# Kernel optimization log

Hardware: AMD Instinct MI355X
Metric: run time of the kernel (lower is better)

The kernel has to match this reference:

```python
import jax, jax.numpy as jnp
import numpy as np

BINS = 10
LOSS_WEIGHT = 1.0


def setup_inputs() -> dict:
    key = jax.random.key(0)
    k1, k2 = jax.random.split(key)
    B, N = 32, 500000
    pred = jax.random.normal(k1, (B, N), dtype=jnp.float32)
    target = jax.random.randint(k2, (B, N), 0, 2).astype(jnp.float32)
    return {"pred": pred, "target": target}


def reference(pred, target):
    bins = BINS
    # edges = [0, 1/bins, ..., 1], last edge bumped by 1e-6 so g==1 falls in last bin
    edges = jnp.arange(bins + 1, dtype=jnp.float32) / bins
    edges = edges.at[-1].add(1e-6)
    tot = target.shape[1]  # python int, matches target.size(1)

    # gradient magnitude proxy; pred.sigmoid() is detached in the original
    g = jnp.abs(jax.lax.stop_gradient(jax.nn.sigmoid(pred)) - jax.lax.stop_gradient(target))

    # single-pass binning replacing the per-bin python loop:
    # inds_i = (g >= edges[i]) & (g < edges[i+1])  <=>  searchsorted(edges, g, 'right') - 1 == i
    idx = jnp.clip(jnp.searchsorted(edges, g.ravel(), side="right") - 1, 0, bins - 1)
    counts = jnp.bincount(idx, length=bins)  # [bins] int
    n = jnp.sum(counts > 0)                  # number of non-empty bins

    cnt_per_elem = counts[idx].astype(pred.dtype)  # count of the bin each element falls in (>=1)
    w = tot / cnt_per_elem                          # weights[inds] = tot / num_in_bins
    w = jnp.where(n > 0, w / n.astype(pred.dtype), w)
    w = jax.lax.stop_gradient(w.reshape(pred.shape))

    # weighted BCE-with-logits, stable form, reduction='sum', divided by tot
    x = pred
    bce = jnp.maximum(x, 0.0) - x * target + jnp.log1p(jnp.exp(-jnp.abs(x)))
    loss = jnp.sum(w * bce) / tot
    return loss * LOSS_WEIGHT
```

## Files before the change

### kernel.cpp

```cpp
#include <hip/hip_runtime.h>
#include <hip/hip_fp16.h>

#define BINS 10

typedef float f32x4 __attribute__((ext_vector_type(4)));

__device__ __forceinline__ unsigned pk_add_f16x2(unsigned a, unsigned b) {
    __half2 ha = __builtin_bit_cast(__half2, a);
    __half2 hb = __builtin_bit_cast(__half2, b);
    return __builtin_bit_cast(unsigned, __hadd2(ha, hb));
}

__device__ __forceinline__ void ghm_elem(float x, float tt,
                                         unsigned long long& pk,
                                         unsigned (&acc)[5]) {
    float t = __expf(-fabsf(x));
    float u = 1.f + t;
    float r = __builtin_amdgcn_rcpf(u);
    float sig = (x >= 0.f) ? r : t * r;
    float d = sig - tt;
    int idx = (int)(fabsf(d) * 10.f);
    idx = idx < 9 ? idx : 9;
    pk += 1ull << (6 * idx);
    float bce = fmaxf(x, 0.f) - x * tt + __logf(u);
    unsigned hv = (unsigned)__builtin_bit_cast(unsigned short, __float2half(bce));
    hv <<= ((idx & 1) << 4);
    const int pair = idx >> 1;
#pragma unroll
    for (int p = 0; p < 5; ++p)
        acc[p] = pk_add_f16x2(acc[p], (pair == p) ? hv : 0u);
}

__global__ __launch_bounds__(256) void ghm_pass1(
    const float* __restrict__ pred, const float* __restrict__ tgt,
    long long n, int nb,
    float* __restrict__ bsum, int* __restrict__ bcnt)
{
    __shared__ float rsum[4][BINS];
    __shared__ int   rcnt[4][BINS];

    const int tid  = threadIdx.x;
    const int lane = tid & 63;
    const int wave = tid >> 6;

    float s[BINS];
#pragma unroll
    for (int b = 0; b < BINS; ++b) s[b] = 0.f;
    unsigned acc[5];
#pragma unroll
    for (int p = 0; p < 5; ++p) acc[p] = 0u;
    unsigned long long pk = 0;
    int c[BINS];
#pragma unroll
    for (int b = 0; b < BINS; ++b) c[b] = 0;

    const long long n4 = n >> 2;
    const f32x4* p4 = (const f32x4*)pred;
    const f32x4* t4 = (const f32x4*)tgt;

    const long long qpb = (n4 + nb - 1) / nb;
    const long long q0  = (long long)blockIdx.x * qpb;
    const long long q1  = (q0 + qpb < n4) ? (q0 + qpb) : n4;

    int chunk = 0;
    for (long long i = q0 + tid; i < q1; i += 512) {
        f32x4 pa = __builtin_nontemporal_load(&p4[i]);
        f32x4 ta = __builtin_nontemporal_load(&t4[i]);
        const long long j = i + 256;
        f32x4 pb, tb;
        const bool has2 = (j < q1);
        if (has2) {
            pb = __builtin_nontemporal_load(&p4[j]);
            tb = __builtin_nontemporal_load(&t4[j]);
        }
        ghm_elem(pa.x, ta.x, pk, acc);
        ghm_elem(pa.y, ta.y, pk, acc);
        ghm_elem(pa.z, ta.z, pk, acc);
        ghm_elem(pa.w, ta.w, pk, acc);
        if (has2) {
            ghm_elem(pb.x, tb.x, pk, acc);
            ghm_elem(pb.y, tb.y, pk, acc);
            ghm_elem(pb.z, tb.z, pk, acc);
            ghm_elem(pb.w, tb.w, pk, acc);
        }
        if (++chunk == 7) {
            chunk = 0;
#pragma unroll
            for (int b = 0; b < BINS; ++b) c[b] += (int)((pk >> (6 * b)) & 63u);
            pk = 0;
#pragma unroll
            for (int p = 0; p < 5; ++p) {
                __half2 h = __builtin_bit_cast(__half2, acc[p]);
                s[2 * p]     += __half2float(__low2half(h));
                s[2 * p + 1] += __half2float(__high2half(h));
                acc[p] = 0u;
            }
        }
    }
    const long long tail0 = n4 << 2;
    if (blockIdx.x == 0 && (long long)tid < (n - tail0))
        ghm_elem(pred[tail0 + tid], tgt[tail0 + tid], pk, acc);
#pragma unroll
    for (int b = 0; b < BINS; ++b) c[b] += (int)((pk >> (6 * b)) & 63u);
#pragma unroll
    for (int p = 0; p < 5; ++p) {
        __half2 h = __builtin_bit_cast(__half2, acc[p]);
        s[2 * p]     += __half2float(__low2half(h));
        s[2 * p + 1] += __half2float(__high2half(h));
    }

#pragma unroll
    for (int b = 0; b < BINS; ++b) {
        float v = s[b];
        int   k = c[b];
        for (int off = 32; off; off >>= 1) {
            v += __shfl_down(v, off);
            k += __shfl_down(k, off);
        }
        if (lane == 0) { rsum[wave][b] = v; rcnt[wave][b] = k; }
    }
    __syncthreads();
    if (tid < BINS) {
        int b = tid;
        float v = rsum[0][b] + rsum[1][b] + rsum[2][b] + rsum[3][b];
        int   k = rcnt[0][b] + rcnt[1][b] + rcnt[2][b] + rcnt[3][b];
        bsum[(long long)b * nb + blockIdx.x] = v;
        bcnt[(long long)b * nb + blockIdx.x] = k;
    }
}

__global__ __launch_bounds__(640) void ghm_pass2(
    const float* __restrict__ bsum, const int* __restrict__ bcnt,
    int nb, float* __restrict__ out)
{
    __shared__ double    ssum[BINS];
    __shared__ long long scnt[BINS];
    const int lane = threadIdx.x & 63;
    const int wave = threadIdx.x >> 6;

    double    acc = 0.0;
    long long cc  = 0;
    for (int i = lane; i < nb; i += 64) {
        acc += (double)bsum[(long long)wave * nb + i];
        cc  += (long long)bcnt[(long long)wave * nb + i];
    }
    for (int off = 32; off; off >>= 1) {
        acc += __shfl_down(acc, off);
        cc  += __shfl_down(cc, off);
    }
    if (lane == 0) { ssum[wave] = acc; scnt[wave] = cc; }
    __syncthreads();

    if (threadIdx.x == 0) {
        int n = 0;
#pragma unroll
        for (int b = 0; b < BINS; ++b) n += (scnt[b] > 0) ? 1 : 0;
        double loss = 0.0;
        if (n > 0) {
#pragma unroll
            for (int b = 0; b < BINS; ++b)
                if (scnt[b] > 0)
                    loss += ssum[b] / ((double)scnt[b] * (double)n);
        }
        out[0] = (float)loss;
    }
}

extern "C" void kernel_launch(void* const* d_in, const int* in_sizes, int n_in,
                              void* d_out, int out_size, void* d_ws, size_t ws_size,
                              hipStream_t stream) {
    const float* pred = (const float*)d_in[0];
    const float* tgt  = (const float*)d_in[1];
    float* out = (float*)d_out;
    const long long n = (long long)in_sizes[0];

    int nb = 2048;
    const size_t per_block = (size_t)BINS * (sizeof(float) + sizeof(int));
    while (nb > 1 && (size_t)nb * per_block > ws_size) nb >>= 1;

    float* bsum = (float*)d_ws;
    int*   bcnt = (int*)((char*)d_ws + (size_t)nb * BINS * sizeof(float));

    ghm_pass1<<<nb, 256, 0, stream>>>(pred, tgt, n, nb, bsum, bcnt);
    ghm_pass2<<<1, 640, 0, stream>>>(bsum, bcnt, nb, out);
}
```

Measured before the change: 44.61 us.

## Switch to grid-stride coalesced loads with software prefetch and single packed count

Replaces the per-block contiguous partition with a grid-stride layout, so consecutive blocks read adjacent memory. It adds a register double-buffer that issues the next pair of vector loads before computing the current pair. When each thread handles at most 60 elements, the 6-bit packed bin counters cannot overflow, so the periodic count flush is dropped. A safe fallback kernel keeps periodic flushes for larger inputs. The cost is higher register pressure and a host-side branch between the two kernels.

```diff
diff --git a/kernel.cpp b/kernel.cpp
--- a/kernel.cpp
+++ b/kernel.cpp
@@ -31,7 +31,21 @@
         acc[p] = pk_add_f16x2(acc[p], (pair == p) ? hv : 0u);
 }
 
-__global__ __launch_bounds__(256) void ghm_pass1(
+#define GHM_QUAD(P, T) do { \
+    ghm_elem((P).x, (T).x, pk, acc); \
+    ghm_elem((P).y, (T).y, pk, acc); \
+    ghm_elem((P).z, (T).z, pk, acc); \
+    ghm_elem((P).w, (T).w, pk, acc); } while (0)
+
+#define GHM_FLUSH_ACC do { \
+    _Pragma("unroll") \
+    for (int p = 0; p < 5; ++p) { \
+        __half2 h = __builtin_bit_cast(__half2, acc[p]); \
+        s[2 * p]     += __half2float(__low2half(h)); \
+        s[2 * p + 1] += __half2float(__high2half(h)); \
+        acc[p] = 0u; } } while (0)
+
+__global__ __launch_bounds__(256) void ghm_pass1_fast(
     const float* __restrict__ pred, const float* __restrict__ tgt,
     long long n, int nb,
     float* __restrict__ bsum, int* __restrict__ bcnt)
@@ -50,65 +64,110 @@
 #pragma unroll
     for (int p = 0; p < 5; ++p) acc[p] = 0u;
     unsigned long long pk = 0;
-    int c[BINS];
-#pragma unroll
-    for (int b = 0; b < BINS; ++b) c[b] = 0;
 
     const long long n4 = n >> 2;
     const f32x4* p4 = (const f32x4*)pred;
     const f32x4* t4 = (const f32x4*)tgt;
 
-    const long long qpb = (n4 + nb - 1) / nb;
-    const long long q0  = (long long)blockIdx.x * qpb;
-    const long long q1  = (q0 + qpb < n4) ? (q0 + qpb) : n4;
-
+    const long long S  = (long long)nb * 256;
+    const long long S2 = S * 2;
+    long long ip = (long long)blockIdx.x * 256 + tid;
     int chunk = 0;
-    for (long long i = q0 + tid; i < q1; i += 512) {
-        f32x4 pa = __builtin_nontemporal_load(&p4[i]);
-        f32x4 ta = __builtin_nontemporal_load(&t4[i]);
-        const long long j = i + 256;
-        f32x4 pb, tb;
-        const bool has2 = (j < q1);
-        if (has2) {
-            pb = __builtin_nontemporal_load(&p4[j]);
-            tb = __builtin_nontemporal_load(&t4[j]);
-        }
-        ghm_elem(pa.x, ta.x, pk, acc);
-        ghm_elem(pa.y, ta.y, pk, acc);
-        ghm_elem(pa.z, ta.z, pk, acc);
-        ghm_elem(pa.w, ta.w, pk, acc);
-        if (has2) {
-            ghm_elem(pb.x, tb.x, pk, acc);
-            ghm_elem(pb.y, tb.y, pk, acc);
-            ghm_elem(pb.z, tb.z, pk, acc);
-            ghm_elem(pb.w, tb.w, pk, acc);
-        }
-        if (++chunk == 7) {
-            chunk = 0;
-#pragma unroll
-            for (int b = 0; b < BINS; ++b) c[b] += (int)((pk >> (6 * b)) & 63u);
-            pk = 0;
-#pragma unroll
-            for (int p = 0; p < 5; ++p) {
-                __half2 h = __builtin_bit_cast(__half2, acc[p]);
-                s[2 * p]     += __half2float(__low2half(h));
-                s[2 * p + 1] += __half2float(__high2half(h));
-                acc[p] = 0u;
-            }
-        }
+
+    if (ip + S < n4) {
+        f32x4 cp0 = __builtin_nontemporal_load(&p4[ip]);
+        f32x4 ct0 = __builtin_nontemporal_load(&t4[ip]);
+        f32x4 cp1 = __builtin_nontemporal_load(&p4[ip + S]);
+        f32x4 ct1 = __builtin_nontemporal_load(&t4[ip + S]);
+        long long nx = ip + S2;
+        while (nx + S < n4) {
+            f32x4 a0 = __builtin_nontemporal_load(&p4[nx]);
+            f32x4 b0 = __builtin_nontemporal_load(&t4[nx]);
+            f32x4 a1 = __builtin_nontemporal_load(&p4[nx + S]);
+            f32x4 b1 = __builtin_nontemporal_load(&t4[nx + S]);
+            GHM_QUAD(cp0, ct0);
+            GHM_QUAD(cp1, ct1);
+            if (++chunk == 7) { chunk = 0; GHM_FLUSH_ACC; }
+            cp0 = a0; ct0 = b0; cp1 = a1; ct1 = b1;
+            nx += S2;
+        }
+        GHM_QUAD(cp0, ct0);
+        GHM_QUAD(cp1, ct1);
+        ip = nx;
+    }
+    for (; ip < n4; ip += S) {
+        f32x4 p = __builtin_nontemporal_load(&p4[ip]);
+        f32x4 t = __builtin_nontemporal_load(&t4[ip]);
+        GHM_QUAD(p, t);
     }
     const long long tail0 = n4 << 2;
     if (blockIdx.x == 0 && (long long)tid < (n - tail0))
         ghm_elem(pred[tail0 + tid], tgt[tail0 + tid], pk, acc);
+    GHM_FLUSH_ACC;
+
+#pragma unroll
+    for (int b = 0; b < BINS; ++b) {
+        float v = s[b];
+        int   k = (int)((pk >> (6 * b)) & 63u);
+        for (int off = 32; off; off >>= 1) {
+            v += __shfl_down(v, off);
+            k += __shfl_down(k, off);
+        }
+        if (lane == 0) { rsum[wave][b] = v; rcnt[wave][b] = k; }
+    }
+    __syncthreads();
+    if (tid < BINS) {
+        int b = tid;
+        float v = rsum[0][b] + rsum[1][b] + rsum[2][b] + rsum[3][b];
+        int   k = rcnt[0][b] + rcnt[1][b] + rcnt[2][b] + rcnt[3][b];
+        bsum[(long long)b * nb + blockIdx.x] = v;
+        bcnt[(long long)b * nb + blockIdx.x] = k;
+    }
+}
+
+__global__ __launch_bounds__(256) void ghm_pass1_safe(
+    const float* __restrict__ pred, const float* __restrict__ tgt,
+    long long n, int nb,
+    float* __restrict__ bsum, int* __restrict__ bcnt)
+{
+    __shared__ float rsum[4][BINS];
+    __shared__ int   rcnt[4][BINS];
+    const int tid  = threadIdx.x;
+    const int lane = tid & 63;
+    const int wave = tid >> 6;
+    float s[BINS];
+#pragma unroll
+    for (int b = 0; b < BINS; ++b) s[b] = 0.f;
+    unsigned acc[5];
+#pragma unroll
+    for (int p = 0; p < 5; ++p) acc[p] = 0u;
+    unsigned long long pk = 0;
+    int c[BINS];
+#pragma unroll
+    for (int b = 0; b < BINS; ++b) c[b] = 0;
+    const long long n4 = n >> 2;
+    const f32x4* p4 = (const f32x4*)pred;
+    const f32x4* t4 = (const f32x4*)tgt;
+    const long long stride = (long long)nb * 256;
+    int chunk = 0;
+    for (long long i = (long long)blockIdx.x * 256 + tid; i < n4; i += stride) {
+        f32x4 p = __builtin_nontemporal_load(&p4[i]);
+        f32x4 t = __builtin_nontemporal_load(&t4[i]);
+        GHM_QUAD(p, t);
+        if (++chunk == 14) {
+            chunk = 0;
+#pragma unroll
+            for (int b = 0; b < BINS; ++b) c[b] += (int)((pk >> (6 * b)) & 63u);
+            pk = 0;
+            GHM_FLUSH_ACC;
+        }
+    }
+    const long long tail0 = n4 << 2;
+    if (blockIdx.x == 0 && (long long)tid < (n - tail0))
+        ghm_elem(pred[tail0 + tid], tgt[tail0 + tid], pk, acc);
 #pragma unroll
     for (int b = 0; b < BINS; ++b) c[b] += (int)((pk >> (6 * b)) & 63u);
-#pragma unroll
-    for (int p = 0; p < 5; ++p) {
-        __half2 h = __builtin_bit_cast(__half2, acc[p]);
-        s[2 * p]     += __half2float(__low2half(h));
-        s[2 * p + 1] += __half2float(__high2half(h));
-    }
-
+    GHM_FLUSH_ACC;
 #pragma unroll
     for (int b = 0; b < BINS; ++b) {
         float v = s[b];
@@ -181,6 +240,13 @@
     float* bsum = (float*)d_ws;
     int*   bcnt = (int*)((char*)d_ws + (size_t)nb * BINS * sizeof(float));
 
-    ghm_pass1<<<nb, 256, 0, stream>>>(pred, tgt, n, nb, bsum, bcnt);
+    const long long n4 = n >> 2;
+    const long long S  = (long long)nb * 256;
+    const long long maxElems = 4 * ((n4 + S - 1) / S) + 4;
+
+    if (maxElems <= 60)
+        ghm_pass1_fast<<<nb, 256, 0, stream>>>(pred, tgt, n, nb, bsum, bcnt);
+    else
+        ghm_pass1_safe<<<nb, 256, 0, stream>>>(pred, tgt, n, nb, bsum, bcnt);
     ghm_pass2<<<1, 640, 0, stream>>>(bsum, bcnt, nb, out);
 }
```

After: 46.08 us. 3.3% more time.
